# Performance work log

Hardware: AMD Instinct MI355X
Metric: run time of the kernel (lower is better)

Reference implementation:

```python
import jax, jax.numpy as jnp
import numpy as np
import math

B, S, D, H = 2, 2048, 1024, 16
HD = D // H
EPS = 1e-05


def gelu(x):
    # tanh-approx GELU as in the torch source
    return 0.5 * x * (1.0 + jnp.tanh(jnp.sqrt(2.0 / jnp.pi) * (x + 0.044715 * x ** 3)))


def layernorm(x, w, b):
    # NOTE: torch .std() uses Bessel correction (ddof=1) and eps is added to std
    u = jnp.mean(x, axis=-1, keepdims=True)
    xc = x - u
    s = jnp.sqrt(jnp.sum(xc * xc, axis=-1, keepdims=True) / (x.shape[-1] - 1))
    return w * (xc / (s + EPS)) + b


def setup_inputs() -> dict:
    key = jax.random.key(0)
    ks = jax.random.split(key, 8)
    std = 0.02
    # weights stored [in, out] (transposed vs torch Linear) so y = x @ W + b
    return {
        "x": jax.random.normal(ks[0], (B, S, D), jnp.float32),
        "ln1_w": jnp.ones((D,), jnp.float32),
        "ln1_b": jnp.zeros((D,), jnp.float32),
        "c_attn_w": jax.random.normal(ks[1], (D, 3 * D), jnp.float32) * std,
        "c_attn_b": jnp.zeros((3 * D,), jnp.float32),
        "c_proj_w": jax.random.normal(ks[2], (D, D), jnp.float32) * std,
        "c_proj_b": jnp.zeros((D,), jnp.float32),
        "ln2_w": jnp.ones((D,), jnp.float32),
        "ln2_b": jnp.zeros((D,), jnp.float32),
        "fc_w": jax.random.normal(ks[3], (D, 4 * D), jnp.float32) * std,
        "fc_b": jnp.zeros((4 * D,), jnp.float32),
        "proj_w": jax.random.normal(ks[4], (4 * D, D), jnp.float32) * std,
        "proj_b": jnp.zeros((D,), jnp.float32),
    }


def attention(x, c_attn_w, c_attn_b, c_proj_w, c_proj_b):
    qkv = x @ c_attn_w + c_attn_b                      # [B,S,3D]
    q, k, v = jnp.split(qkv, 3, axis=-1)
    q = q.reshape(B, S, H, HD)
    k = k.reshape(B, S, H, HD)
    v = v.reshape(B, S, H, HD)
    w = jnp.einsum("bqhd,bkhd->bhqk", q, k) / math.sqrt(HD)  # scale=True
    bias = jnp.tril(jnp.ones((S, S), jnp.float32))     # causal mask
    w = w * bias - 1e10 * (1.0 - bias)
    w = jax.nn.softmax(w, axis=-1)
    a = jnp.einsum("bhqk,bkhd->bqhd", w, v).reshape(B, S, D)
    return a @ c_proj_w + c_proj_b


def reference(x, ln1_w, ln1_b, c_attn_w, c_attn_b, c_proj_w, c_proj_b,
              ln2_w, ln2_b, fc_w, fc_b, proj_w, proj_b):
    a = attention(layernorm(x, ln1_w, ln1_b), c_attn_w, c_attn_b, c_proj_w, c_proj_b)
    x = x + a
    h = gelu(layernorm(x, ln2_w, ln2_b) @ fc_w + fc_b)
    m = h @ proj_w + proj_b
    return x + m
```

## Files before the change

kernel.cpp:

```cpp
#include <hip/hip_runtime.h>

typedef unsigned short u16;
typedef __attribute__((ext_vector_type(8))) short short8;
typedef __attribute__((ext_vector_type(4))) float floatx4;

__device__ __forceinline__ float bf2f(u16 u) {
  unsigned int v = ((unsigned int)u) << 16;
  return __builtin_bit_cast(float, v);
}
__device__ __forceinline__ u16 f2bf(float f) {
  unsigned int u = __builtin_bit_cast(unsigned int, f);
  u += 0x7FFFu + ((u >> 16) & 1u);
  return (u16)(u >> 16);
}
__device__ __forceinline__ void gload_lds16(const void* g, void* l) {
  __builtin_amdgcn_global_load_lds(
      (const __attribute__((address_space(1))) unsigned int*)g,
      (__attribute__((address_space(3))) unsigned int*)l, 16, 0, 0);
}

__global__ __launch_bounds__(256) void transpose_f32_bf16(const float* __restrict__ in,
                                                          u16* __restrict__ out,
                                                          int K, int N) {
  __shared__ float tile[32][33];
  int n0 = blockIdx.x * 32, k0 = blockIdx.y * 32;
  int tx = threadIdx.x & 31, ty = threadIdx.x >> 5;
#pragma unroll
  for (int i = 0; i < 4; i++) {
    int r = ty + i * 8;
    tile[r][tx] = in[(size_t)(k0 + r) * N + n0 + tx];
  }
  __syncthreads();
#pragma unroll
  for (int i = 0; i < 4; i++) {
    int r = ty + i * 8;
    out[(size_t)(n0 + r) * K + k0 + tx] = f2bf(tile[tx][r]);
  }
}

__global__ __launch_bounds__(256) void ln_f32(const float* __restrict__ xin,
                                              const float* __restrict__ wgt,
                                              const float* __restrict__ bia,
                                              u16* __restrict__ out) {
  int row = blockIdx.x, t = threadIdx.x;
  const float* xr = xin + (size_t)row * 1024 + t * 4;
  float4 f = *(const float4*)xr;
  float v[4] = {f.x, f.y, f.z, f.w};
  float s1 = v[0] + v[1] + v[2] + v[3];
  float s2 = v[0] * v[0] + v[1] * v[1] + v[2] * v[2] + v[3] * v[3];
#pragma unroll
  for (int off = 32; off; off >>= 1) {
    s1 += __shfl_down(s1, off);
    s2 += __shfl_down(s2, off);
  }
  __shared__ float red[8];
  int lane = t & 63, w = t >> 6;
  if (lane == 0) { red[w] = s1; red[4 + w] = s2; }
  __syncthreads();
  s1 = red[0] + red[1] + red[2] + red[3];
  s2 = red[4] + red[5] + red[6] + red[7];
  float mean = s1 * (1.f / 1024.f);
  float var = (s2 - 1024.f * mean * mean) * (1.f / 1023.f);
  var = var < 0.f ? 0.f : var;
  float inv = 1.f / (sqrtf(var) + 1e-5f);
  float4 wv = *(const float4*)(wgt + t * 4);
  float4 bv = *(const float4*)(bia + t * 4);
  float wa[4] = {wv.x, wv.y, wv.z, wv.w};
  float ba[4] = {bv.x, bv.y, bv.z, bv.w};
#pragma unroll
  for (int j = 0; j < 4; j++)
    out[(size_t)row * 1024 + t * 4 + j] = f2bf(wa[j] * ((v[j] - mean) * inv) + ba[j]);
}

template <int EPI>
__global__ __launch_bounds__(256) void gemm_bt(const u16* __restrict__ A,
                                               const u16* __restrict__ Bt,
                                               const float* __restrict__ bias,
                                               const float* __restrict__ res,
                                               void* __restrict__ outp,
                                               void* __restrict__ outp2,
                                               int msplit,
                                               int ldc, int K) {
  __shared__ __align__(16) u16 As[128 * 64];
  __shared__ __align__(16) u16 Bs[128 * 64];
  int tid = threadIdx.x;
  int lane = tid & 63, w = tid >> 6;
  int quad = lane >> 4, c16 = lane & 15;
  int wm = w >> 1, wn = w & 1;
  int nbx = gridDim.x;
  int nwg = nbx * gridDim.y;
  int bid = blockIdx.y * nbx + blockIdx.x;
  int swz = (bid & 7) * (nwg >> 3) + (bid >> 3);
  int bn = swz % nbx, bm = swz / nbx;
  const u16* Ab = A + (size_t)bm * 128 * K;
  const u16* Bb = Bt + (size_t)bn * 128 * K;

  int rbase = tid >> 3;
  int csrc = (((tid & 7) ^ ((tid >> 3) & 7))) * 8;
  int dbase = w * 512;

  floatx4 zf = {0.f, 0.f, 0.f, 0.f};
  floatx4 acc[4][4];
#pragma unroll
  for (int i = 0; i < 4; i++)
#pragma unroll
    for (int j = 0; j < 4; j++) acc[i][j] = zf;

  auto stage = [&](int kt) {
    const u16* At = Ab + kt * 64;
    const u16* Bt2 = Bb + kt * 64;
#pragma unroll
    for (int j = 0; j < 4; j++) {
      int r = j * 32 + rbase;
      gload_lds16(At + (size_t)r * K + csrc, &As[j * 2048 + dbase]);
      gload_lds16(Bt2 + (size_t)r * K + csrc, &Bs[j * 2048 + dbase]);
    }
  };

  int nt = K >> 6;
  for (int t = 0; t < nt; ++t) {
    stage(t);
    asm volatile("s_waitcnt vmcnt(0)" ::: "memory");
    __builtin_amdgcn_s_barrier();
    __builtin_amdgcn_sched_barrier(0);
#pragma unroll
    for (int ks = 0; ks < 2; ++ks) {
      int col = (ks * 32 + quad * 8) ^ ((c16 & 7) * 8);
      short8 af[4], bfr[4];
#pragma unroll
      for (int mt = 0; mt < 4; mt++)
        af[mt] = *(const short8*)&As[(wm * 64 + mt * 16 + c16) * 64 + col];
#pragma unroll
      for (int nt2 = 0; nt2 < 4; nt2++)
        bfr[nt2] = *(const short8*)&Bs[(wn * 64 + nt2 * 16 + c16) * 64 + col];
#pragma unroll
      for (int mt = 0; mt < 4; mt++)
#pragma unroll
        for (int nt2 = 0; nt2 < 4; nt2++)
          acc[mt][nt2] = __builtin_amdgcn_mfma_f32_16x16x32_bf16(af[mt], bfr[nt2], acc[mt][nt2], 0, 0, 0);
    }
    __builtin_amdgcn_s_barrier();
    __builtin_amdgcn_sched_barrier(0);
  }

  int gm0 = bm * 128 + wm * 64;
  int gn0 = bn * 128 + wn * 64;
#pragma unroll
  for (int nt2 = 0; nt2 < 4; nt2++) {
    int gn = gn0 + nt2 * 16 + c16;
    float bia = 0.f;
    if constexpr (EPI != 3) bia = bias[gn];
#pragma unroll
    for (int mt = 0; mt < 4; mt++) {
#pragma unroll
      for (int r = 0; r < 4; r++) {
        int gm = gm0 + mt * 16 + quad * 4 + r;
        float v = acc[mt][nt2][r] + bia;
        if constexpr (EPI == 0) {
          void* op = outp;
          int gmo = gm;
          if (gm >= msplit) { op = outp2; gmo = gm - msplit; }
          ((u16*)op)[(size_t)gmo * ldc + gn] = f2bf(v);
        } else if constexpr (EPI == 1) {
          size_t o = (size_t)gm * ldc + gn;
          ((float*)outp)[o] = v + res[o];
        } else if constexpr (EPI == 2) {
          size_t o = (size_t)gm * ldc + gn;
          float y = 0.7978845608f * (v + 0.044715f * v * v * v);
          float g = v / (1.f + __expf(-2.f * y));
          ((u16*)outp)[o] = f2bf(g);
        } else {
          size_t o = (size_t)gm * ldc + gn;
          ((float*)outp)[o] += v;
        }
      }
    }
  }
}

template <int EPI>
__global__ __launch_bounds__(512) void gemm_bt2(const u16* __restrict__ A,
                                                const u16* __restrict__ Bt,
                                                const float* __restrict__ bias,
                                                const float* __restrict__ res,
                                                void* __restrict__ outp,
                                                void* __restrict__ outp2,
                                                int msplit,
                                                int ldc, int K) {
  __shared__ __align__(16) u16 As[256 * 64];
  __shared__ __align__(16) u16 Bs[128 * 64];
  int tid = threadIdx.x;
  int lane = tid & 63, w = tid >> 6;
  int quad = lane >> 4, c16 = lane & 15;
  int wm = w >> 1, wn = w & 1;
  int nbx = gridDim.x;
  int nwg = nbx * gridDim.y;
  int bid = blockIdx.y * nbx + blockIdx.x;
  int swz = (bid & 7) * (nwg >> 3) + (bid >> 3);
  int bn = swz % nbx, bm = swz / nbx;
  const u16* Ab = A + (size_t)bm * 256 * K;
  const u16* Bb = Bt + (size_t)bn * 128 * K;

  int rbase = tid >> 3;
  int csrc = (((tid & 7) ^ ((tid >> 3) & 7))) * 8;
  int dbase = w * 512;

  floatx4 zf = {0.f, 0.f, 0.f, 0.f};
  floatx4 acc[4][4];
#pragma unroll
  for (int i = 0; i < 4; i++)
#pragma unroll
    for (int j = 0; j < 4; j++) acc[i][j] = zf;

  auto stage = [&](int kt) {
    const u16* At = Ab + kt * 64;
    const u16* Bt2 = Bb + kt * 64;
#pragma unroll
    for (int j = 0; j < 4; j++)
      gload_lds16(At + (size_t)(j * 64 + rbase) * K + csrc, &As[j * 4096 + dbase]);
#pragma unroll
    for (int j = 0; j < 2; j++)
      gload_lds16(Bt2 + (size_t)(j * 64 + rbase) * K + csrc, &Bs[j * 4096 + dbase]);
  };

  int nt = K >> 6;
  for (int t = 0; t < nt; ++t) {
    stage(t);
    asm volatile("s_waitcnt vmcnt(0)" ::: "memory");
    __builtin_amdgcn_s_barrier();
    __builtin_amdgcn_sched_barrier(0);
#pragma unroll
    for (int ks = 0; ks < 2; ++ks) {
      int col = (ks * 32 + quad * 8) ^ ((c16 & 7) * 8);
      short8 af[4], bfr[4];
#pragma unroll
      for (int mt = 0; mt < 4; mt++)
        af[mt] = *(const short8*)&As[(wm * 64 + mt * 16 + c16) * 64 + col];
#pragma unroll
      for (int nt2 = 0; nt2 < 4; nt2++)
        bfr[nt2] = *(const short8*)&Bs[(wn * 64 + nt2 * 16 + c16) * 64 + col];
#pragma unroll
      for (int mt = 0; mt < 4; mt++)
#pragma unroll
        for (int nt2 = 0; nt2 < 4; nt2++)
          acc[mt][nt2] = __builtin_amdgcn_mfma_f32_16x16x32_bf16(af[mt], bfr[nt2], acc[mt][nt2], 0, 0, 0);
    }
    __builtin_amdgcn_s_barrier();
    __builtin_amdgcn_sched_barrier(0);
  }

  int gm0 = bm * 256 + wm * 64;
  int gn0 = bn * 128 + wn * 64;
#pragma unroll
  for (int nt2 = 0; nt2 < 4; nt2++) {
    int gn = gn0 + nt2 * 16 + c16;
    float bia = 0.f;
    if constexpr (EPI != 3) bia = bias[gn];
#pragma unroll
    for (int mt = 0; mt < 4; mt++) {
#pragma unroll
      for (int r = 0; r < 4; r++) {
        int gm = gm0 + mt * 16 + quad * 4 + r;
        float v = acc[mt][nt2][r] + bia;
        if constexpr (EPI == 0) {
          void* op = outp;
          int gmo = gm;
          if (gm >= msplit) { op = outp2; gmo = gm - msplit; }
          ((u16*)op)[(size_t)gmo * ldc + gn] = f2bf(v);
        } else if constexpr (EPI == 1) {
          size_t o = (size_t)gm * ldc + gn;
          ((float*)outp)[o] = v + res[o];
        } else if constexpr (EPI == 2) {
          size_t o = (size_t)gm * ldc + gn;
          float y = 0.7978845608f * (v + 0.044715f * v * v * v);
          float g = v / (1.f + __expf(-2.f * y));
          ((u16*)outp)[o] = f2bf(g);
        } else {
          size_t o = (size_t)gm * ldc + gn;
          ((float*)outp)[o] += v;
        }
      }
    }
  }
}

__device__ __forceinline__ void attn_process(
    const short8& qf0, const short8& qf1,
    float* m_run, float* l_run, floatx4* oacc,
    const u16* __restrict__ Ks, const u16* __restrict__ Vt, u16* __restrict__ pw,
    int kt, int qt, int wrow, int quad, int c16, bool diag) {
  floatx4 zf = {0.f, 0.f, 0.f, 0.f};
  floatx4 s[4];
#pragma unroll
  for (int n = 0; n < 4; n++) {
    short8 kf0 = *(const short8*)&Ks[(n * 16 + c16) * 72 + quad * 8];
    short8 kf1 = *(const short8*)&Ks[(n * 16 + c16) * 72 + 32 + quad * 8];
    floatx4 a = zf;
    a = __builtin_amdgcn_mfma_f32_16x16x32_bf16(qf0, kf0, a, 0, 0, 0);
    a = __builtin_amdgcn_mfma_f32_16x16x32_bf16(qf1, kf1, a, 0, 0, 0);
    s[n] = a;
  }
  if (diag) {
#pragma unroll
    for (int n = 0; n < 4; n++) {
      int kg = kt * 64 + n * 16 + c16;
#pragma unroll
      for (int r = 0; r < 4; r++) {
        int qg = qt * 64 + wrow * 16 + quad * 4 + r;
        s[n][r] = (kg > qg) ? -1e30f : s[n][r];
      }
    }
  }
  float mt[4];
#pragma unroll
  for (int r = 0; r < 4; r++)
    mt[r] = fmaxf(fmaxf(s[0][r], s[1][r]), fmaxf(s[2][r], s[3][r]));
#pragma unroll
  for (int off = 1; off < 16; off <<= 1)
#pragma unroll
    for (int r = 0; r < 4; r++) mt[r] = fmaxf(mt[r], __shfl_xor(mt[r], off));
  float alpha[4], lsum[4];
#pragma unroll
  for (int r = 0; r < 4; r++) {
    float mn = fmaxf(m_run[r], mt[r]);
    alpha[r] = __expf(m_run[r] - mn);
    m_run[r] = mn;
    lsum[r] = 0.f;
  }
#pragma unroll
  for (int n = 0; n < 4; n++)
#pragma unroll
    for (int r = 0; r < 4; r++) {
      float p = __expf(s[n][r] - m_run[r]);
      s[n][r] = p;
      lsum[r] += p;
    }
#pragma unroll
  for (int off = 1; off < 16; off <<= 1)
#pragma unroll
    for (int r = 0; r < 4; r++) lsum[r] += __shfl_xor(lsum[r], off);
#pragma unroll
  for (int r = 0; r < 4; r++) l_run[r] = l_run[r] * alpha[r] + lsum[r];
#pragma unroll
  for (int c = 0; c < 4; c++)
#pragma unroll
    for (int r = 0; r < 4; r++) oacc[c][r] *= alpha[r];
#pragma unroll
  for (int n = 0; n < 4; n++)
#pragma unroll
    for (int r = 0; r < 4; r++)
      pw[(quad * 4 + r) * 72 + n * 16 + c16] = f2bf(s[n][r]);
  short8 pf0 = *(const short8*)&pw[c16 * 72 + quad * 8];
  short8 pf1 = *(const short8*)&pw[c16 * 72 + 32 + quad * 8];
#pragma unroll
  for (int c = 0; c < 4; c++) {
    int d = c * 16 + c16;
    int cd = (d & 56) ^ ((d & 7) << 3);
    short8 vf0 = *(const short8*)&Vt[d * 64 + ((quad * 8) ^ cd)];
    short8 vf1 = *(const short8*)&Vt[d * 64 + ((32 + quad * 8) ^ cd)];
    oacc[c] = __builtin_amdgcn_mfma_f32_16x16x32_bf16(pf0, vf0, oacc[c], 0, 0, 0);
    oacc[c] = __builtin_amdgcn_mfma_f32_16x16x32_bf16(pf1, vf1, oacc[c], 0, 0, 0);
  }
}

__device__ __forceinline__ short8 scale8_eighth(short8 v) {
  short8 r;
#pragma unroll
  for (int j = 0; j < 8; j++) {
    unsigned int b = ((unsigned int)(u16)v[j]) << 16;
    float f = __builtin_bit_cast(float, b) * 0.125f;
    r[j] = (short)(u16)(__builtin_bit_cast(unsigned int, f) >> 16);
  }
  return r;
}

__global__ __launch_bounds__(512) void attn_mfma2(const u16* __restrict__ qkv0,
                                                  const u16* __restrict__ qkv1,
                                                  u16* __restrict__ aout) {
  int pr = blockIdx.x, h = blockIdx.y;
  const u16* qkvb = blockIdx.z ? qkv1 : qkv0;
  aout += (size_t)blockIdx.z * 2048 * 1024;
  int qt0 = pr, qt1 = 31 - pr;
  int tid = threadIdx.x, lane = tid & 63, w = tid >> 6;
  int quad = lane >> 4, c16 = lane & 15;
  int wrow = w & 3, tb = w >> 2;
  int qt_my = tb ? qt0 : qt1;
  __shared__ __align__(16) u16 Ks[2][64 * 72];
  __shared__ __align__(16) u16 Vt[2][64 * 64];
  __shared__ __align__(16) u16 Ps[8][16 * 72];

  size_t qoff = (size_t)(qt_my * 64 + wrow * 16 + c16) * 3072 + h * 64;
  short8 qf0 = scale8_eighth(*(const short8*)(qkvb + qoff + quad * 8));
  short8 qf1 = scale8_eighth(*(const short8*)(qkvb + qoff + 32 + quad * 8));

  floatx4 zf = {0.f, 0.f, 0.f, 0.f};
  float m[4], l[4];
  floatx4 o[4];
#pragma unroll
  for (int r = 0; r < 4; r++) { m[r] = -1e30f; l[r] = 0.f; }
#pragma unroll
  for (int c = 0; c < 4; c++) o[c] = zf;

  int srow = tid >> 3;
  int sd8 = (tid & 7) * 8;
  short8 kr, vr;

  auto issue = [&](int kt) {
    size_t gb = (size_t)(kt * 64 + srow) * 3072 + h * 64 + sd8;
    kr = *(const short8*)(qkvb + gb + 1024);
    vr = *(const short8*)(qkvb + gb + 2048);
  };
  auto commit = [&](int b) {
    *(short8*)&Ks[b][srow * 72 + sd8] = kr;
    u16* vt = Vt[b];
#pragma unroll
    for (int j = 0; j < 8; j++) {
      int d = sd8 + j;
      vt[d * 64 + (srow ^ (d & 56) ^ ((d & 7) << 3))] = (u16)vr[j];
    }
  };

  u16* pw = &Ps[w][0];
  issue(0);
  commit(0);
  __syncthreads();
  int cur = 0;
  for (int kt = 0; kt <= qt1; ++kt) {
    if (kt < qt1) issue(kt + 1);

    if (tb == 0 || kt <= qt0)
      attn_process(qf0, qf1, m, l, o, Ks[cur], Vt[cur], pw, kt, qt_my, wrow,
                   quad, c16, kt == qt_my);

    if (kt < qt1) {
      commit(cur ^ 1);
      __syncthreads();
      cur ^= 1;
    }
  }

  size_t ob = (size_t)(qt_my * 64 + wrow * 16) * 1024 + h * 64;
#pragma unroll
  for (int r = 0; r < 4; r++) {
    float inv = 1.f / l[r];
#pragma unroll
    for (int c = 0; c < 4; c++)
      aout[ob + (size_t)(quad * 4 + r) * 1024 + c * 16 + c16] = f2bf(o[c][r] * inv);
  }
}

extern "C" void kernel_launch(void* const* d_in, const int* in_sizes, int n_in,
                              void* d_out, int out_size, void* d_ws, size_t ws_size,
                              hipStream_t stream) {
  const float* x        = (const float*)d_in[0];
  const float* ln1_w    = (const float*)d_in[1];
  const float* ln1_b    = (const float*)d_in[2];
  const float* c_attn_w = (const float*)d_in[3];
  const float* c_attn_b = (const float*)d_in[4];
  const float* c_proj_w = (const float*)d_in[5];
  const float* c_proj_b = (const float*)d_in[6];
  const float* ln2_w    = (const float*)d_in[7];
  const float* ln2_b    = (const float*)d_in[8];
  const float* fc_w     = (const float*)d_in[9];
  const float* fc_b     = (const float*)d_in[10];
  const float* proj_w   = (const float*)d_in[11];
  const float* proj_b   = (const float*)d_in[12];

  char* ws = (char*)d_ws;
  const size_t MiB = 1u << 20;
  const int BIG = 1 << 30;

  u16* wt_attn  = (u16*)(ws + 0);
  u16* wt_cproj = (u16*)(ws + 6 * MiB);
  u16* ln1b     = (u16*)(ws + 8 * MiB);
  u16* qkv1     = (u16*)(ws + 16 * MiB);
  u16* qkv0     = (u16*)d_out;
  u16* attn_out = (u16*)(ws + 8 * MiB);
  float* x1     = (float*)d_out;

  transpose_f32_bf16<<<dim3(96, 32), 256, 0, stream>>>(c_attn_w, wt_attn, 1024, 3072);
  transpose_f32_bf16<<<dim3(32, 32), 256, 0, stream>>>(c_proj_w, wt_cproj, 1024, 1024);
  ln_f32<<<4096, 256, 0, stream>>>(x, ln1_w, ln1_b, ln1b);
  gemm_bt2<0><<<dim3(24, 16), 512, 0, stream>>>(ln1b, wt_attn, c_attn_b, nullptr,
                                                qkv0, qkv1, 2048, 3072, 1024);
  attn_mfma2<<<dim3(16, 16, 2), 512, 0, stream>>>(qkv0, qkv1, attn_out);
  gemm_bt<1><<<dim3(8, 32), 256, 0, stream>>>(attn_out, wt_cproj, c_proj_b, x,
                                              x1, nullptr, BIG, 1024, 1024);

  int NC = (ws_size >= 58720256) ? 1 : (ws_size >= 37748736) ? 2 : 4;
  int CN = 4096 / NC;
  u16* wt_fc = (u16*)(ws + 0);
  u16* ln2b  = (u16*)(ws + 8 * MiB);
  u16* h_c   = (u16*)(ws + 16 * MiB);
  u16* projT = (u16*)(ws + 16 * MiB + (size_t)4096 * CN * 2);

  transpose_f32_bf16<<<dim3(128, 32), 256, 0, stream>>>(fc_w, wt_fc, 1024, 4096);
  ln_f32<<<4096, 256, 0, stream>>>(x1, ln2_w, ln2_b, ln2b);
  for (int c = 0; c < NC; c++) {
    transpose_f32_bf16<<<dim3(32, CN / 32), 256, 0, stream>>>(
        proj_w + (size_t)c * CN * 1024, projT, CN, 1024);
    if (CN >= 2048)
      gemm_bt2<2><<<dim3(CN / 128, 16), 512, 0, stream>>>(
          ln2b, wt_fc + (size_t)c * CN * 1024, fc_b + c * CN, nullptr,
          h_c, nullptr, BIG, CN, 1024);
    else
      gemm_bt<2><<<dim3(CN / 128, 32), 256, 0, stream>>>(
          ln2b, wt_fc + (size_t)c * CN * 1024, fc_b + c * CN, nullptr,
          h_c, nullptr, BIG, CN, 1024);
    if (NC == 1)
      gemm_bt<1><<<dim3(8, 32), 256, 0, stream>>>(h_c, projT, proj_b, x1,
                                                  x1, nullptr, BIG, 1024, CN);
    else if (c < NC - 1)
      gemm_bt<3><<<dim3(8, 32), 256, 0, stream>>>(h_c, projT, nullptr, nullptr,
                                                  x1, nullptr, BIG, 1024, CN);
    else
      gemm_bt<4><<<dim3(8, 32), 256, 0, stream>>>(h_c, projT, proj_b, nullptr,
                                                  x1, nullptr, BIG, 1024, CN);
  }
}
```

Before: 357.4 us.

## Use lazy softmax rescaling and compute row sums via MFMA with ones

The flash-attention inner step now rescales the running max, output accumulator and row sum only when some row's tile max exceeds the running max by more than 8 (checked wave-wide with __any). The per-row sum of probabilities, previously built with a shuffle reduction, is now computed by two MFMAs multiplying the bf16 P fragment by a vector of ones. This removes shuffles and rescale multiplies from the per-tile critical path. In exchange it adds two MFMAs per tile, the sum is taken over bf16-rounded probabilities, and exponentials can reach up to e^8 before a rescale.

```diff
diff --git a/kernel.cpp b/kernel.cpp
--- a/kernel.cpp
+++ b/kernel.cpp
@@ -286,7 +286,7 @@
 
 __device__ __forceinline__ void attn_process(
     const short8& qf0, const short8& qf1,
-    float* m_run, float* l_run, floatx4* oacc,
+    float* m_run, floatx4& lacc, floatx4* oacc,
     const u16* __restrict__ Ks, const u16* __restrict__ Vt, u16* __restrict__ pw,
     int kt, int qt, int wrow, int quad, int c16, bool diag) {
   floatx4 zf = {0.f, 0.f, 0.f, 0.f};
@@ -319,32 +319,25 @@
   for (int off = 1; off < 16; off <<= 1)
 #pragma unroll
     for (int r = 0; r < 4; r++) mt[r] = fmaxf(mt[r], __shfl_xor(mt[r], off));
-  float alpha[4], lsum[4];
-#pragma unroll
-  for (int r = 0; r < 4; r++) {
-    float mn = fmaxf(m_run[r], mt[r]);
-    alpha[r] = __expf(m_run[r] - mn);
-    m_run[r] = mn;
-    lsum[r] = 0.f;
+  bool need = false;
+#pragma unroll
+  for (int r = 0; r < 4; r++) need |= (mt[r] > m_run[r] + 8.f);
+  if (__any(need)) {
+#pragma unroll
+    for (int r = 0; r < 4; r++) {
+      float mn = fmaxf(m_run[r], mt[r]);
+      float alpha = __expf(m_run[r] - mn);
+      m_run[r] = mn;
+      lacc[r] *= alpha;
+#pragma unroll
+      for (int c = 0; c < 4; c++) oacc[c][r] *= alpha;
+    }
   }
 #pragma unroll
   for (int n = 0; n < 4; n++)
 #pragma unroll
-    for (int r = 0; r < 4; r++) {
-      float p = __expf(s[n][r] - m_run[r]);
-      s[n][r] = p;
-      lsum[r] += p;
-    }
-#pragma unroll
-  for (int off = 1; off < 16; off <<= 1)
-#pragma unroll
-    for (int r = 0; r < 4; r++) lsum[r] += __shfl_xor(lsum[r], off);
-#pragma unroll
-  for (int r = 0; r < 4; r++) l_run[r] = l_run[r] * alpha[r] + lsum[r];
-#pragma unroll
-  for (int c = 0; c < 4; c++)
-#pragma unroll
-    for (int r = 0; r < 4; r++) oacc[c][r] *= alpha[r];
+    for (int r = 0; r < 4; r++)
+      s[n][r] = __expf(s[n][r] - m_run[r]);
 #pragma unroll
   for (int n = 0; n < 4; n++)
 #pragma unroll
@@ -352,6 +345,11 @@
       pw[(quad * 4 + r) * 72 + n * 16 + c16] = f2bf(s[n][r]);
   short8 pf0 = *(const short8*)&pw[c16 * 72 + quad * 8];
   short8 pf1 = *(const short8*)&pw[c16 * 72 + 32 + quad * 8];
+  short8 ones;
+#pragma unroll
+  for (int j = 0; j < 8; j++) ones[j] = (short)0x3F80;
+  lacc = __builtin_amdgcn_mfma_f32_16x16x32_bf16(pf0, ones, lacc, 0, 0, 0);
+  lacc = __builtin_amdgcn_mfma_f32_16x16x32_bf16(pf1, ones, lacc, 0, 0, 0);
 #pragma unroll
   for (int c = 0; c < 4; c++) {
     int d = c * 16 + c16;
@@ -394,10 +392,12 @@
   short8 qf1 = scale8_eighth(*(const short8*)(qkvb + qoff + 32 + quad * 8));
 
   floatx4 zf = {0.f, 0.f, 0.f, 0.f};
-  float m[4], l[4];
+  float m[4];
+  floatx4 lacc;
   floatx4 o[4];
 #pragma unroll
-  for (int r = 0; r < 4; r++) { m[r] = -1e30f; l[r] = 0.f; }
+  for (int r = 0; r < 4; r++) m[r] = -1e30f;
+  lacc = zf;
 #pragma unroll
   for (int c = 0; c < 4; c++) o[c] = zf;
 
@@ -429,7 +429,7 @@
     if (kt < qt1) issue(kt + 1);
 
     if (tb == 0 || kt <= qt0)
-      attn_process(qf0, qf1, m, l, o, Ks[cur], Vt[cur], pw, kt, qt_my, wrow,
+      attn_process(qf0, qf1, m, lacc, o, Ks[cur], Vt[cur], pw, kt, qt_my, wrow,
                    quad, c16, kt == qt_my);
 
     if (kt < qt1) {
@@ -442,7 +442,7 @@
   size_t ob = (size_t)(qt_my * 64 + wrow * 16) * 1024 + h * 64;
 #pragma unroll
   for (int r = 0; r < 4; r++) {
-    float inv = 1.f / l[r];
+    float inv = 1.f / lacc[r];
 #pragma unroll
     for (int c = 0; c < 4; c++)
       aout[ob + (size_t)(quad * 4 + r) * 1024 + c * 16 + c16] = f2bf(o[c][r] * inv);
```

Result: no change. 351.2 us (-1.7%).
